# Kernel tuning notes

Measured on AMD Instinct MI355X. Metric: run time of the kernel, lower is better.

The kernel has to match this reference:

```python
import jax, jax.numpy as jnp
import numpy as np

B, T, DIM, H = 32, 1024, 512, 8
HD = DIM // H
HID = int(DIM * 4.0)
EPS = 1e-6
SCALE = HD ** -0.5


def _ln(t, g, b):
    m = t.mean(-1, keepdims=True)
    var = ((t - m) ** 2).mean(-1, keepdims=True)
    return (t - m) * jax.lax.rsqrt(var + EPS) * g + b


def setup_inputs() -> dict:
    key = jax.random.key(0)
    ks = jax.random.split(key, 10)
    n = lambda k, s: jax.random.normal(k, s, dtype=jnp.float32)
    w = lambda k, s: n(k, s) * 0.02
    z = lambda d: jnp.zeros((d,), dtype=jnp.float32)
    o = lambda d: jnp.ones((d,), dtype=jnp.float32)
    return {
        'x': n(ks[0], (B, T, DIM)),
        'k': n(ks[1], (T, H, B, HD)),
        'v': n(ks[2], (T, H, B, HD)),
        'Wqkv': w(ks[3], (DIM, 3 * DIM)), 'bqkv': z(3 * DIM),
        'Wsa': w(ks[4], (DIM, DIM)), 'bsa': z(DIM),
        'Wq': w(ks[5], (DIM, DIM)), 'bq': z(DIM),
        'Wed': w(ks[6], (DIM, DIM)), 'bed': z(DIM),
        'g1': o(DIM), 'be1': z(DIM),
        'g2': o(DIM), 'be2': z(DIM),
        'g3': o(DIM), 'be3': z(DIM),
        'W1': w(ks[7], (DIM, HID)), 'b1': z(HID),
        'W2': w(ks[8], (HID, DIM)), 'b2': z(DIM),
    }


def _decoder_block(x, k, v, Wqkv, bqkv, Wsa, bsa, Wq, bq, Wed, bed,
                   g1, be1, g2, be2, g3, be3, W1, b1, W2, b2):
    # ---- self-attention (faithful to the original, degenerate einsums) ----
    qkv = x @ Wqkv + bqkv                                        # [B,T,3*DIM]
    qkv = qkv.reshape(B, T, 3, H, HD).transpose(2, 1, 3, 0, 4)   # [3,T,H,B,HD]
    q, sk, sv = qkv[0], qkv[1], qkv[2]
    dp = jnp.einsum('kabc,qdef->qabe', sk, q) * SCALE            # [T,H,B,B]
    scores = jax.nn.softmax(dp, axis=-1)
    wa = jnp.einsum('qabc,kdef->bqaf', scores, sv).reshape(B, T, DIM)
    attn = wa @ Wsa + bsa
    an1 = _ln(attn + x, g1, be1)
    # ---- encoder-decoder attention ----
    qe = (an1 @ Wq + bq).reshape(B, T, H, HD).transpose(1, 2, 0, 3)  # [T,H,B,HD]
    dp2 = jnp.einsum('abkd,abqd->abqk', k, qe) * SCALE           # [T,H,B,B]
    sc2 = jax.nn.softmax(dp2, axis=-1)
    wa2 = jnp.einsum('abts,abse->tabe', sc2, v).reshape(B, T, DIM)
    attn2 = wa2 @ Wed + bed
    an2 = _ln(attn2 + x, g2, be2)
    # ---- MLP (exact GELU, as nn.GELU default) ----
    hmid = jax.nn.gelu(an2 @ W1 + b1, approximate=False)
    z = hmid @ W2 + b2
    return _ln(z + an2, g3, be3)


def reference(x, k, v, Wqkv, bqkv, Wsa, bsa, Wq, bq, Wed, bed,
              g1, be1, g2, be2, g3, be3, W1, b1, W2, b2):
    return _decoder_block(x, k, v, Wqkv, bqkv, Wsa, bsa, Wq, bq, Wed, bed,
                          g1, be1, g2, be2, g3, be3, W1, b1, W2, b2)
```

## Files before the change

### kernel.cpp

```cpp
#include <hip/hip_runtime.h>
#include <hip/hip_bf16.h>
#include <math.h>

#define Bn 32
#define Tn 1024
#define DIMn 512
#define Hn 8
#define HDn 64
#define HIDn 2048
#define Mn 32768

using short8 = __attribute__((ext_vector_type(8))) short;
using half8  = __attribute__((ext_vector_type(8))) _Float16;
using f32x4  = __attribute__((ext_vector_type(4))) float;
typedef unsigned short u16;
typedef unsigned int   u32;

__device__ __forceinline__ u16 f2h(float x) {
  _Float16 h = (_Float16)x;
  return __builtin_bit_cast(u16, h);
}
__device__ __forceinline__ float h2f(u16 u) {
  return (float)__builtin_bit_cast(_Float16, u);
}
__device__ __forceinline__ u32 pack2h(float a, float b) {
  return (u32)f2h(a) | ((u32)f2h(b) << 16);
}
__device__ __forceinline__ void gld16(const void* g, void* l) {
  __builtin_amdgcn_global_load_lds((const __attribute__((address_space(1))) u32*)g,
                                   (__attribute__((address_space(3))) u32*)l, 16, 0, 0);
}
__device__ __forceinline__ float wredsum(float v) {
  #pragma unroll
  for (int d = 1; d < 64; d <<= 1) v += __shfl_xor(v, d, 64);
  return v;
}
__device__ __forceinline__ float fast_gelu(float v) {
  const float ax = fabsf(v) * 0.70710678118654752f;
  const float t = 1.0f / (1.0f + 0.3275911f * ax);
  const float p = ((((1.061405429f * t - 1.453152027f) * t) + 1.421413741f) * t - 0.284496736f) * t + 0.254829592f;
  const float y = 1.0f - p * t * __expf(-ax * ax);
  const float erfv = (v >= 0.f) ? y : -y;
  return 0.5f * v * (1.0f + erfv);
}

__global__ __launch_bounds__(256) void colsum1(const float* __restrict__ x, float* __restrict__ part) {
  const int b = blockIdx.x, t = threadIdx.x;
  const float* p = x + (size_t)b * 128 * DIMn;
  float a0 = 0.f, a1 = 0.f;
  for (int r = 0; r < 128; ++r) {
    a0 += p[r * DIMn + t];
    a1 += p[r * DIMn + t + 256];
  }
  part[b * DIMn + t] = a0;
  part[b * DIMn + t + 256] = a1;
}

__global__ __launch_bounds__(256) void colsum2(const float* __restrict__ part, float* __restrict__ xs) {
  const int c = blockIdx.x * 256 + threadIdx.x;
  float a = 0.f;
  for (int b = 0; b < 256; ++b) a += part[b * DIMn + c];
  xs[c] = a;
}

__global__ __launch_bounds__(256) void sv_k(const float* __restrict__ xs, const float* __restrict__ Wqkv,
                                            const float* __restrict__ bqkv, float* __restrict__ SVp) {
  __shared__ float xsh[512];
  __shared__ float red[4][64];
  const int h = blockIdx.x, q = threadIdx.x >> 6, f = threadIdx.x & 63;
  xsh[threadIdx.x] = xs[threadIdx.x];
  xsh[threadIdx.x + 256] = xs[threadIdx.x + 256];
  __syncthreads();
  const int colb = 2 * DIMn + h * HDn + f;
  float acc = 0.f;
  for (int i = q * 128; i < q * 128 + 128; ++i) acc += xsh[i] * Wqkv[(size_t)i * 1536 + colb];
  red[q][f] = acc;
  __syncthreads();
  if (q == 0)
    SVp[h * 64 + f] = red[0][f] + red[1][f] + red[2][f] + red[3][f] + 32768.0f * bqkv[colb];
}

__global__ __launch_bounds__(256) void attnc2_k(const float* __restrict__ SVp, const float* __restrict__ Wsa,
                                                const float* __restrict__ bsa, float* __restrict__ attnc) {
  __shared__ float SVs[64];
  __shared__ float red[4][64];
  const int q = threadIdx.x >> 6, jj = threadIdx.x & 63;
  if (threadIdx.x < 64) {
    float s = 0.f;
    #pragma unroll
    for (int h = 0; h < 8; ++h) s += SVp[h * 64 + threadIdx.x];
    SVs[threadIdx.x] = s;
  }
  __syncthreads();
  const int j = blockIdx.x * 64 + jj;
  float acc = 0.f;
  for (int i = q * 128; i < q * 128 + 128; ++i) acc += SVs[i & 63] * Wsa[(size_t)i * DIMn + j];
  red[q][jj] = acc;
  __syncthreads();
  if (q == 0) attnc[j] = red[0][jj] + red[1][jj] + red[2][jj] + red[3][jj] + bsa[j];
}

__global__ __launch_bounds__(256) void wtrans(const float* __restrict__ W, u16* __restrict__ WT, int K, int N) {
  __shared__ float tile[64][65];
  const int n0 = blockIdx.x * 64, k0 = blockIdx.y * 64;
  const int t = threadIdx.x;
  #pragma unroll
  for (int i = 0; i < 16; ++i) {
    const int fl = i * 256 + t, r = fl >> 6, c = fl & 63;
    tile[r][c] = W[(size_t)(k0 + r) * N + n0 + c];
  }
  __syncthreads();
  #pragma unroll
  for (int i = 0; i < 16; ++i) {
    const int fl = i * 256 + t, r = fl >> 6, c = fl & 63;
    WT[(size_t)(n0 + r) * K + k0 + c] = f2h(tile[c][r]);
  }
}

template <int MODE>
__global__ __launch_bounds__(256) void ln_k(const void* __restrict__ Ap, const void* __restrict__ Bp,
                                            const float* __restrict__ cv, const float* __restrict__ g,
                                            const float* __restrict__ be, void* __restrict__ outp) {
  const int row = blockIdx.x * 4 + (threadIdx.x >> 6);
  const int l = threadIdx.x & 63;
  const size_t base = (size_t)row * DIMn + l * 8;
  float v[8];
  if (MODE == 0 || MODE == 2) {
    const float* a = (const float*)Ap + base;
    float4 x0 = *(const float4*)a;
    float4 x1 = *(const float4*)(a + 4);
    v[0] = x0.x; v[1] = x0.y; v[2] = x0.z; v[3] = x0.w;
    v[4] = x1.x; v[5] = x1.y; v[6] = x1.z; v[7] = x1.w;
  } else {
    short8 s = *(const short8*)((const u16*)Ap + base);
    #pragma unroll
    for (int i = 0; i < 8; ++i) v[i] = h2f((u16)s[i]);
  }
  if (MODE == 0) {
    float4 c0 = *(const float4*)(cv + l * 8);
    float4 c1 = *(const float4*)(cv + l * 8 + 4);
    v[0] += c0.x; v[1] += c0.y; v[2] += c0.z; v[3] += c0.w;
    v[4] += c1.x; v[5] += c1.y; v[6] += c1.z; v[7] += c1.w;
  } else if (MODE == 1) {
    const float* b = (const float*)Bp + base;
    float4 x0 = *(const float4*)b;
    float4 x1 = *(const float4*)(b + 4);
    v[0] += x0.x; v[1] += x0.y; v[2] += x0.z; v[3] += x0.w;
    v[4] += x1.x; v[5] += x1.y; v[6] += x1.z; v[7] += x1.w;
  } else {
    short8 s2 = *(const short8*)((const u16*)Bp + base);
    #pragma unroll
    for (int i = 0; i < 8; ++i) v[i] += h2f((u16)s2[i]);
  }
  float s = 0.f;
  #pragma unroll
  for (int i = 0; i < 8; ++i) s += v[i];
  s = wredsum(s);
  const float mean = s * (1.0f / 512.0f);
  float q = 0.f;
  #pragma unroll
  for (int i = 0; i < 8; ++i) { const float d = v[i] - mean; q += d * d; }
  q = wredsum(q);
  const float rs = rsqrtf(q * (1.0f / 512.0f) + 1e-6f);
  float gg[8], bb[8];
  {
    float4 g0 = *(const float4*)(g + l * 8);
    float4 g1 = *(const float4*)(g + l * 8 + 4);
    float4 b0 = *(const float4*)(be + l * 8);
    float4 b1 = *(const float4*)(be + l * 8 + 4);
    gg[0] = g0.x; gg[1] = g0.y; gg[2] = g0.z; gg[3] = g0.w;
    gg[4] = g1.x; gg[5] = g1.y; gg[6] = g1.z; gg[7] = g1.w;
    bb[0] = b0.x; bb[1] = b0.y; bb[2] = b0.z; bb[3] = b0.w;
    bb[4] = b1.x; bb[5] = b1.y; bb[6] = b1.z; bb[7] = b1.w;
  }
  float y[8];
  #pragma unroll
  for (int i = 0; i < 8; ++i) y[i] = (v[i] - mean) * rs * gg[i] + bb[i];
  if (MODE == 2) {
    float* o = (float*)outp + base;
    *(float4*)o = make_float4(y[0], y[1], y[2], y[3]);
    *(float4*)(o + 4) = make_float4(y[4], y[5], y[6], y[7]);
  } else {
    short8 o;
    #pragma unroll
    for (int i = 0; i < 8; ++i) o[i] = (short)f2h(y[i]);
    *(short8*)((u16*)outp + base) = o;
  }
}

#define CPAD 132
template <bool GELU, bool OBF>
__global__ __launch_bounds__(256) void gemm_bt(const u16* __restrict__ A, const u16* __restrict__ BT,
                                               const float* __restrict__ bias, u16* __restrict__ OB,
                                               float* __restrict__ OF, int Ni, int Ki, int gridX) {
  __shared__ u16 As[128 * 32];
  __shared__ u16 Bs[128 * 32];
  __shared__ u16 Cs[128 * CPAD];
  const int tid = threadIdx.x;
  const int l = tid & 63, w = tid >> 6, wr = w >> 1, wc = w & 1;

  int wg = blockIdx.x;
  const int nwg = gridDim.x;
  if ((nwg & 7) == 0) {
    const int q = nwg >> 3;
    wg = (wg & 7) * q + (wg >> 3);
  }
  const int bx = wg % gridX, by = wg / gridX;
  const int m0 = by * 128, n0 = bx * 128;
  const int r16 = l & 15, g4 = l >> 4;

  const u16* ga = A + (size_t)(m0 + (tid >> 2)) * (size_t)Ki + (tid & 3) * 8;
  const u16* gb = BT + (size_t)(n0 + (tid >> 2)) * (size_t)Ki + (tid & 3) * 8;
  const int ldst = tid * 8;

  int aoff[4], boff[4];
  #pragma unroll
  for (int i = 0; i < 4; ++i) {
    aoff[i] = (wr * 64 + i * 16 + r16) * 32 + g4 * 8;
    boff[i] = (wc * 64 + i * 16 + r16) * 32 + g4 * 8;
  }
  f32x4 acc[4][4] = {};

  for (int k0 = 0; k0 < Ki; k0 += 32) {
    gld16(ga + k0, &As[ldst]);
    gld16(ga + k0 + (size_t)64 * Ki, &As[ldst + 2048]);
    gld16(gb + k0, &Bs[ldst]);
    gld16(gb + k0 + (size_t)64 * Ki, &Bs[ldst + 2048]);
    __syncthreads();
    half8 af[4], bf[4];
    #pragma unroll
    for (int i = 0; i < 4; ++i) af[i] = *(const half8*)&As[aoff[i]];
    #pragma unroll
    for (int i = 0; i < 4; ++i) bf[i] = *(const half8*)&Bs[boff[i]];
    #pragma unroll
    for (int mi = 0; mi < 4; ++mi)
      #pragma unroll
      for (int ni = 0; ni < 4; ++ni)
        acc[mi][ni] = __builtin_amdgcn_mfma_f32_16x16x32_f16(af[mi], bf[ni], acc[mi][ni], 0, 0, 0);
    __syncthreads();
  }

  if (OBF) {
    #pragma unroll
    for (int ni = 0; ni < 4; ++ni) {
      const int col = wc * 64 + ni * 16 + r16;
      const float bv = bias[n0 + col];
      #pragma unroll
      for (int mi = 0; mi < 4; ++mi) {
        const int rowb = wr * 64 + mi * 16 + g4 * 4;
        #pragma unroll
        for (int r = 0; r < 4; ++r) {
          float v = acc[mi][ni][r] + bv;
          if (GELU) v = fast_gelu(v);
          Cs[(rowb + r) * CPAD + col] = f2h(v);
        }
      }
    }
    __syncthreads();
    const int rr = tid >> 4;
    const int c0 = (tid & 15) * 8;
    #pragma unroll
    for (int j = 0; j < 8; ++j) {
      const int row = rr + j * 16;
      *(short8*)(OB + (size_t)(m0 + row) * Ni + n0 + c0) = *(const short8*)&Cs[row * CPAD + c0];
    }
  } else {
    #pragma unroll
    for (int ni = 0; ni < 4; ++ni) {
      const int col = n0 + wc * 64 + ni * 16 + r16;
      const float bv = bias[col];
      #pragma unroll
      for (int mi = 0; mi < 4; ++mi) {
        const int rowb = m0 + wr * 64 + mi * 16 + g4 * 4;
        #pragma unroll
        for (int r = 0; r < 4; ++r) {
          float v = acc[mi][ni][r] + bv;
          if (GELU) v = fast_gelu(v);
          OF[(size_t)(rowb + r) * Ni + col] = v;
        }
      }
    }
  }
}

__global__ __launch_bounds__(64) void attn_k(const u16* __restrict__ qe, const float* __restrict__ kin,
                                             const float* __restrict__ vin, u16* __restrict__ wa2) {
  const int t = blockIdx.x >> 3;
  const int h = blockIdx.x & 7;
  const int l = threadIdx.x;
  __shared__ u16 Kq[32 * 80];
  __shared__ u16 Qq[32 * 80];
  __shared__ u16 VT[64 * 48];
  __shared__ u16 Ps[32 * 48];

  const float* kp = kin + (size_t)blockIdx.x * 2048;
  const float* vp = vin + (size_t)blockIdx.x * 2048;
  #pragma unroll
  for (int i = 0; i < 8; ++i) {
    const int fl = i * 256 + l * 4;
    const int r = fl >> 6, c = fl & 63;
    float4 kv = *(const float4*)(kp + fl);
    float4 vv = *(const float4*)(vp + fl);
    *(u32*)&Kq[r * 80 + c]     = pack2h(kv.x, kv.y);
    *(u32*)&Kq[r * 80 + c + 2] = pack2h(kv.z, kv.w);
    VT[(c + 0) * 48 + r] = f2h(vv.x);
    VT[(c + 1) * 48 + r] = f2h(vv.y);
    VT[(c + 2) * 48 + r] = f2h(vv.z);
    VT[(c + 3) * 48 + r] = f2h(vv.w);
  }
  {
    const int qb = l >> 1, hf = l & 1;
    const u16* qp = qe + (size_t)(qb * Tn + t) * DIMn + h * HDn + hf * 32;
    #pragma unroll
    for (int j = 0; j < 4; ++j) {
      short8 d = *(const short8*)(qp + j * 8);
      *(short8*)&Qq[qb * 80 + hf * 32 + j * 8] = d;
    }
  }
  __syncthreads();

  const int r16 = l & 15, g4 = l >> 4;
  f32x4 sacc[2][2] = {};
  #pragma unroll
  for (int kk = 0; kk < 2; ++kk) {
    half8 aQ0 = *(const half8*)&Qq[r16 * 80 + kk * 32 + g4 * 8];
    half8 aQ1 = *(const half8*)&Qq[(16 + r16) * 80 + kk * 32 + g4 * 8];
    half8 bK0 = *(const half8*)&Kq[r16 * 80 + kk * 32 + g4 * 8];
    half8 bK1 = *(const half8*)&Kq[(16 + r16) * 80 + kk * 32 + g4 * 8];
    sacc[0][0] = __builtin_amdgcn_mfma_f32_16x16x32_f16(aQ0, bK0, sacc[0][0], 0, 0, 0);
    sacc[0][1] = __builtin_amdgcn_mfma_f32_16x16x32_f16(aQ0, bK1, sacc[0][1], 0, 0, 0);
    sacc[1][0] = __builtin_amdgcn_mfma_f32_16x16x32_f16(aQ1, bK0, sacc[1][0], 0, 0, 0);
    sacc[1][1] = __builtin_amdgcn_mfma_f32_16x16x32_f16(aQ1, bK1, sacc[1][1], 0, 0, 0);
  }
  #pragma unroll
  for (int m = 0; m < 2; ++m) {
    #pragma unroll
    for (int r = 0; r < 4; ++r) {
      const float a0 = sacc[m][0][r] * 0.125f;
      const float a1 = sacc[m][1][r] * 0.125f;
      float mx = fmaxf(a0, a1);
      #pragma unroll
      for (int d = 1; d < 16; d <<= 1) mx = fmaxf(mx, __shfl_xor(mx, d, 64));
      const float e0 = __expf(a0 - mx), e1 = __expf(a1 - mx);
      float sm = e0 + e1;
      #pragma unroll
      for (int d = 1; d < 16; d <<= 1) sm += __shfl_xor(sm, d, 64);
      const float inv = 1.0f / sm;
      const int rr = m * 16 + g4 * 4 + r;
      Ps[rr * 48 + r16]      = f2h(e0 * inv);
      Ps[rr * 48 + 16 + r16] = f2h(e1 * inv);
    }
  }
  __syncthreads();

  half8 aP0 = *(const half8*)&Ps[r16 * 48 + g4 * 8];
  half8 aP1 = *(const half8*)&Ps[(16 + r16) * 48 + g4 * 8];
  f32x4 oacc[2][4] = {};
  #pragma unroll
  for (int nn = 0; nn < 4; ++nn) {
    half8 bV = *(const half8*)&VT[(nn * 16 + r16) * 48 + g4 * 8];
    oacc[0][nn] = __builtin_amdgcn_mfma_f32_16x16x32_f16(aP0, bV, oacc[0][nn], 0, 0, 0);
    oacc[1][nn] = __builtin_amdgcn_mfma_f32_16x16x32_f16(aP1, bV, oacc[1][nn], 0, 0, 0);
  }
  #pragma unroll
  for (int m = 0; m < 2; ++m) {
    #pragma unroll
    for (int r = 0; r < 4; ++r) {
      const int qb = m * 16 + g4 * 4 + r;
      u16* op = wa2 + (size_t)(qb * Tn + t) * DIMn + h * HDn;
      #pragma unroll
      for (int nn = 0; nn < 4; ++nn)
        op[nn * 16 + r16] = f2h(oacc[m][nn][r]);
    }
  }
}

extern "C" void kernel_launch(void* const* d_in, const int* in_sizes, int n_in,
                              void* d_out, int out_size, void* d_ws, size_t ws_size,
                              hipStream_t stream) {
  (void)in_sizes; (void)n_in; (void)out_size;
  const float* x    = (const float*)d_in[0];
  const float* kin  = (const float*)d_in[1];
  const float* vin  = (const float*)d_in[2];
  const float* Wqkv = (const float*)d_in[3];
  const float* bqkv = (const float*)d_in[4];
  const float* Wsa  = (const float*)d_in[5];
  const float* bsa  = (const float*)d_in[6];
  const float* Wq   = (const float*)d_in[7];
  const float* bq   = (const float*)d_in[8];
  const float* Wed  = (const float*)d_in[9];
  const float* bed  = (const float*)d_in[10];
  const float* g1   = (const float*)d_in[11];
  const float* be1  = (const float*)d_in[12];
  const float* g2   = (const float*)d_in[13];
  const float* be2  = (const float*)d_in[14];
  const float* g3   = (const float*)d_in[15];
  const float* be3  = (const float*)d_in[16];
  const float* W1   = (const float*)d_in[17];
  const float* b1   = (const float*)d_in[18];
  const float* W2   = (const float*)d_in[19];
  const float* b2   = (const float*)d_in[20];

  char* ws = (char*)d_ws;
  float* xs    = (float*)(ws);
  float* SVp   = (float*)(ws + (2 << 10));
  float* attnc = (float*)(ws + (4 << 10));
  float* part  = (float*)(ws + (6 << 10));
  u16* wqT  = (u16*)(ws + (1 << 20));
  u16* wedT = (u16*)(ws + (1 << 20) + (512 << 10));
  u16* w1T  = (u16*)(ws + (2 << 20));
  u16* w2T  = (u16*)(ws + (4 << 20));
  u16* Abuf = (u16*)(ws + (6 << 20));
  const size_t HOFF = 38ull << 20;
  u16* hmid = (u16*)(ws + HOFF);

  u16* an1  = Abuf;
  u16* wa2  = Abuf;
  u16* an2b = Abuf;
  u16*   qe   = (u16*)d_out;
  u16*   a2bf = (u16*)d_out;
  float* zf   = (float*)d_out;

  long long avail = (long long)ws_size - (long long)HOFF;
  int crows = (avail > 0) ? (int)(avail / (HIDn * 2)) : 128;
  crows = (crows / 128) * 128;
  if (crows < 128) crows = 128;
  if (crows > Mn) crows = Mn;

  colsum1<<<256, 256, 0, stream>>>(x, part);
  colsum2<<<2, 256, 0, stream>>>(part, xs);
  sv_k<<<8, 256, 0, stream>>>(xs, Wqkv, bqkv, SVp);
  attnc2_k<<<8, 256, 0, stream>>>(SVp, Wsa, bsa, attnc);

  wtrans<<<dim3(8, 8),  256, 0, stream>>>(Wq,  wqT,  512, 512);
  wtrans<<<dim3(8, 8),  256, 0, stream>>>(Wed, wedT, 512, 512);
  wtrans<<<dim3(32, 8), 256, 0, stream>>>(W1,  w1T,  512, 2048);
  wtrans<<<dim3(8, 32), 256, 0, stream>>>(W2,  w2T,  2048, 512);

  ln_k<0><<<Mn / 4, 256, 0, stream>>>(x, nullptr, attnc, g1, be1, an1);
  gemm_bt<false, true><<<1024, 256, 0, stream>>>(an1, wqT, bq, qe, nullptr, 512, 512, 4);
  attn_k<<<Tn * Hn, 64, 0, stream>>>(qe, kin, vin, wa2);
  gemm_bt<false, true><<<1024, 256, 0, stream>>>(wa2, wedT, bed, a2bf, nullptr, 512, 512, 4);
  ln_k<1><<<Mn / 4, 256, 0, stream>>>(a2bf, x, nullptr, g2, be2, an2b);
  for (int r0 = 0; r0 < Mn; r0 += crows) {
    int rc = Mn - r0; if (rc > crows) rc = crows;
    gemm_bt<true, true><<<16 * (rc / 128), 256, 0, stream>>>(an2b + (size_t)r0 * DIMn, w1T, b1, hmid, nullptr, HIDn, DIMn, 16);
    gemm_bt<false, false><<<4 * (rc / 128), 256, 0, stream>>>(hmid, w2T, b2, nullptr, zf + (size_t)r0 * DIMn, DIMn, HIDn, 4);
  }
  ln_k<2><<<Mn / 4, 256, 0, stream>>>(zf, an2b, nullptr, g3, be3, d_out);
}
```

Measured before the change: 473.7 us.

## Triple-buffer GEMM LDS tiles with async global_load_lds prefetch two stages ahead

Result: faster. 428.7 us (-9.5%).

```diff
diff --git a/kernel.cpp b/kernel.cpp
--- a/kernel.cpp
+++ b/kernel.cpp
@@ -34,6 +34,11 @@
   #pragma unroll
   for (int d = 1; d < 64; d <<= 1) v += __shfl_xor(v, d, 64);
   return v;
+}
+__device__ __forceinline__ void hard_barrier() {
+  asm volatile("" ::: "memory");
+  __builtin_amdgcn_s_barrier();
+  asm volatile("" ::: "memory");
 }
 __device__ __forceinline__ float fast_gelu(float v) {
   const float ax = fabsf(v) * 0.70710678118654752f;
@@ -193,9 +198,7 @@
 __global__ __launch_bounds__(256) void gemm_bt(const u16* __restrict__ A, const u16* __restrict__ BT,
                                                const float* __restrict__ bias, u16* __restrict__ OB,
                                                float* __restrict__ OF, int Ni, int Ki, int gridX) {
-  __shared__ u16 As[128 * 32];
-  __shared__ u16 Bs[128 * 32];
-  __shared__ u16 Cs[128 * CPAD];
+  __shared__ u16 smem[3 * 8192];
   const int tid = threadIdx.x;
   const int l = tid & 63, w = tid >> 6, wr = w >> 1, wc = w & 1;
 
@@ -217,30 +220,45 @@
   #pragma unroll
   for (int i = 0; i < 4; ++i) {
     aoff[i] = (wr * 64 + i * 16 + r16) * 32 + g4 * 8;
-    boff[i] = (wc * 64 + i * 16 + r16) * 32 + g4 * 8;
+    boff[i] = 4096 + (wc * 64 + i * 16 + r16) * 32 + g4 * 8;
   }
   f32x4 acc[4][4] = {};
 
-  for (int k0 = 0; k0 < Ki; k0 += 32) {
-    gld16(ga + k0, &As[ldst]);
-    gld16(ga + k0 + (size_t)64 * Ki, &As[ldst + 2048]);
-    gld16(gb + k0, &Bs[ldst]);
-    gld16(gb + k0 + (size_t)64 * Ki, &Bs[ldst + 2048]);
-    __syncthreads();
+  const int nt = Ki >> 5;
+  auto STAGE = [&](int t, int b) {
+    u16* base = smem + b * 8192;
+    const int kk = t * 32;
+    gld16(ga + kk, &base[ldst]);
+    gld16(ga + kk + (size_t)64 * Ki, &base[ldst + 2048]);
+    gld16(gb + kk, &base[4096 + ldst]);
+    gld16(gb + kk + (size_t)64 * Ki, &base[4096 + ldst + 2048]);
+  };
+
+  STAGE(0, 0);
+  STAGE(1, 1);
+  int b0 = 0, b1 = 1, b2 = 2;
+  for (int t = 0; t < nt; ++t) {
+    if (t < nt - 1) asm volatile("s_waitcnt vmcnt(4)" ::: "memory");
+    else            asm volatile("s_waitcnt vmcnt(0)" ::: "memory");
+    hard_barrier();
+    if (t + 2 < nt) STAGE(t + 2, b2);
+    const u16* base = smem + b0 * 8192;
     half8 af[4], bf[4];
     #pragma unroll
-    for (int i = 0; i < 4; ++i) af[i] = *(const half8*)&As[aoff[i]];
-    #pragma unroll
-    for (int i = 0; i < 4; ++i) bf[i] = *(const half8*)&Bs[boff[i]];
+    for (int i = 0; i < 4; ++i) af[i] = *(const half8*)&base[aoff[i]];
+    #pragma unroll
+    for (int i = 0; i < 4; ++i) bf[i] = *(const half8*)&base[boff[i]];
     #pragma unroll
     for (int mi = 0; mi < 4; ++mi)
       #pragma unroll
       for (int ni = 0; ni < 4; ++ni)
         acc[mi][ni] = __builtin_amdgcn_mfma_f32_16x16x32_f16(af[mi], bf[ni], acc[mi][ni], 0, 0, 0);
-    __syncthreads();
+    hard_barrier();
+    const int tb = b0; b0 = b1; b1 = b2; b2 = tb;
   }
 
   if (OBF) {
+    u16* Cs = smem;
     #pragma unroll
     for (int ni = 0; ni < 4; ++ni) {
       const int col = wc * 64 + ni * 16 + r16;
@@ -256,7 +274,7 @@
         }
       }
     }
-    __syncthreads();
+    hard_barrier();
     const int rr = tid >> 4;
     const int c0 = (tid & 15) * 8;
     #pragma unroll
```
